# Performance work log

Hardware: AMD Instinct MI355X
Metric: run time of the kernel (lower is better)

The kernel has to match this reference:

```python
import jax, jax.numpy as jnp
import numpy as np

N_NODES = 100000
N_EDGES = 3200000
N_GRAPHS = 64
IN_DIM, OUT_DIM = 16, 3


def _gcn_layer(x, src, dst, ew, W, b, n):
    # PyG GCNConv with edge_weight: transform first, then normalized propagate
    # with added self-loops (weight 1.0). deg_i = sum_{e: dst=i} w_e + 1.
    xw = x @ W  # [N, out]
    deg = jax.ops.segment_sum(ew, dst, num_segments=n) + 1.0  # [N]
    dinv = jax.lax.rsqrt(deg)
    norm = dinv[src] * ew * dinv[dst]  # [E]
    agg = jax.ops.segment_sum(xw[src] * norm[:, None], dst, num_segments=n)
    # self-loop contribution: dinv_i * 1.0 * dinv_i = 1/deg_i
    return agg + xw * (1.0 / deg)[:, None] + b


def setup_inputs() -> dict:
    key = jax.random.key(0)
    ks = jax.random.split(key, 16)
    glorot = lambda k, fi, fo: jax.random.normal(k, (fi, fo), jnp.float32) * jnp.sqrt(2.0 / (fi + fo))
    return {
        "x": jax.random.normal(ks[0], (N_NODES, IN_DIM), jnp.float32),
        "edge_index": jax.random.randint(ks[1], (2, N_EDGES), 0, N_NODES, jnp.int32),
        "edge_attr": jax.random.uniform(ks[2], (N_EDGES,), jnp.float32),
        "batch": jnp.sort(jax.random.randint(ks[3], (N_NODES,), 0, N_GRAPHS, jnp.int32)),
        "W1": glorot(ks[4], IN_DIM, 16), "b1": jnp.zeros((16,), jnp.float32),
        "W2": glorot(ks[5], 16, 64),     "b2": jnp.zeros((64,), jnp.float32),
        "W3": glorot(ks[6], 64, 256),    "b3": jnp.zeros((256,), jnp.float32),
        "L1": glorot(ks[7], 256, 128),   "c1": jnp.zeros((128,), jnp.float32),
        "L2": glorot(ks[8], 128, 64),    "c2": jnp.zeros((64,), jnp.float32),
        "L3": glorot(ks[9], 64, OUT_DIM), "c3": jnp.zeros((OUT_DIM,), jnp.float32),
    }


def reference(x, edge_index, edge_attr, batch, W1, b1, W2, b2, W3, b3, L1, c1, L2, c2, L3, c3):
    src, dst = edge_index[0], edge_index[1]
    h = jax.nn.silu(_gcn_layer(x, src, dst, edge_attr, W1, b1, N_NODES))
    h = jax.nn.silu(_gcn_layer(h, src, dst, edge_attr, W2, b2, N_NODES))
    h = jax.nn.silu(_gcn_layer(h, src, dst, edge_attr, W3, b3, N_NODES))
    # global mean pool per graph
    sums = jax.ops.segment_sum(h, batch, num_segments=N_GRAPHS)  # [G, 256]
    cnt = jax.ops.segment_sum(jnp.ones((N_NODES,), h.dtype), batch, num_segments=N_GRAPHS)
    pooled = sums / jnp.maximum(cnt, 1.0)[:, None]
    z = jax.nn.silu(pooled @ L1 + c1)
    z = jax.nn.silu(z @ L2 + c2)
    z = z @ L3 + c3
    return jnp.squeeze(z)
```

## Files before the change

### kernel.cpp

```cpp
#include <hip/hip_runtime.h>
#include <math.h>


#define NBH 1024
#define POOL_C 8
#define CAP 10240

typedef _Float16 half8 __attribute__((ext_vector_type(8)));
typedef float f32x4 __attribute__((ext_vector_type(4)));

__device__ __forceinline__ float silu_f(float v) { return v / (1.0f + expf(-v)); }

__global__ void k_init(const int* __restrict__ batch, int* __restrict__ bounds,
                       int* __restrict__ btotal, int N, int G) {
    int t = threadIdx.x;
    btotal[t] = 0;
    if (t > G) return;
    if (t == G) { bounds[G] = N; return; }
    int lo = 0, hi = N;
    while (lo < hi) { int m = (lo + hi) >> 1; if (batch[m] < t) lo = m + 1; else hi = m; }
    bounds[t] = lo;
}

__global__ __launch_bounds__(256) void k_bscatter(const int* __restrict__ src,
                                                  const int* __restrict__ dst,
                                                  const float* __restrict__ ew,
                                                  int* __restrict__ btotal,
                                                  int2* __restrict__ ebuf,
                                                  int E, int B, int ept) {
    __shared__ int hist[512];
    __shared__ int cur[512];
    int blk = blockIdx.x, t = threadIdx.x;
    for (int i = t; i < B; i += 256) hist[i] = 0;
    __syncthreads();
    int start = blk * 256 * ept;
    for (int j = 0; j < ept; j++) {
        int e = start + j * 256 + t;
        if (e < E) atomicAdd(&hist[dst[e] >> 8], 1);
    }
    __syncthreads();
    for (int b = t; b < B; b += 256)
        cur[b] = b * CAP + atomicAdd(&btotal[b], hist[b]);
    __syncthreads();
    for (int j = 0; j < ept; j++) {
        int e = start + j * 256 + t;
        if (e < E) {
            int d = dst[e];
            int b = d >> 8;
            int pos = atomicAdd(&cur[b], 1);
            if (pos < (b + 1) * CAP)
                ebuf[pos] = make_int2(src[e] | ((d & 255) << 24), __float_as_int(ew[e]));
        }
    }
}

__global__ __launch_bounds__(256) void k_bucket_csr(const int2* __restrict__ ebuf,
                                                    const int* __restrict__ btotal,
                                                    int2* __restrict__ csr,
                                                    unsigned int* __restrict__ offs,
                                                    float* __restrict__ dinv,
                                                    const float* __restrict__ x,
                                                    _Float16* __restrict__ xp,
                                                    int N) {
    __shared__ int ncnt[256];
    __shared__ int excl[256];
    __shared__ float wsum[256];
    int b = blockIdx.x, t = threadIdx.x;
    int base = b * CAP;
    int end = base + min(btotal[b], CAP);
    ncnt[t] = 0;
    wsum[t] = 0.0f;
    __syncthreads();
    for (int i = base + t; i < end; i += 256)
        atomicAdd(&ncnt[(unsigned)ebuf[i].x >> 24], 1);
    __syncthreads();
    int v = ncnt[t];
    excl[t] = v;
    __syncthreads();
#pragma unroll
    for (int o = 1; o < 256; o <<= 1) {
        int x2 = (t >= o) ? excl[t - o] : 0;
        __syncthreads();
        excl[t] += x2;
        __syncthreads();
    }
    int ex = excl[t] - v;
    int n = (b << 8) + t;
    if (n < N) offs[n] = (unsigned)(base + ex) | ((unsigned)v << 24);
    __syncthreads();
    ncnt[t] = base + ex;
    __syncthreads();
    for (int i = base + t; i < end; i += 256) {
        int2 ent = ebuf[i];
        int node = (unsigned)ent.x >> 24;
        int pos = atomicAdd(&ncnt[node], 1);
        csr[pos] = make_int2(ent.x & 0x00FFFFFF, ent.y);
        atomicAdd(&wsum[node], __int_as_float(ent.y));
    }
    __syncthreads();
    if (n < N) {
        float dv = 1.0f / sqrtf(1.0f + wsum[t]);
        dinv[n] = dv;
        const float4* xr = (const float4*)(x + (long long)n * 16);
        half8* xw = (half8*)(xp + (long long)n * 16);
#pragma unroll
        for (int j = 0; j < 2; j++) {
            float4 a = xr[2 * j], c = xr[2 * j + 1];
            half8 hv;
            hv[0] = (_Float16)(a.x * dv); hv[1] = (_Float16)(a.y * dv);
            hv[2] = (_Float16)(a.z * dv); hv[3] = (_Float16)(a.w * dv);
            hv[4] = (_Float16)(c.x * dv); hv[5] = (_Float16)(c.y * dv);
            hv[6] = (_Float16)(c.z * dv); hv[7] = (_Float16)(c.w * dv);
            xw[j] = hv;
        }
    }
}

__global__ __launch_bounds__(256) void k_gx1(const _Float16* __restrict__ h,
                                             const int2* __restrict__ csr,
                                             const unsigned int* __restrict__ offs,
                                             const float* __restrict__ dinv,
                                             const float* __restrict__ W,
                                             const float* __restrict__ b,
                                             _Float16* __restrict__ out, int N) {
    __shared__ float Ws[16 * 16];
    __shared__ float bs[16];
    if (threadIdx.x < 256) Ws[threadIdx.x] = W[threadIdx.x];
    if (threadIdx.x < 16) bs[threadIdx.x] = b[threadIdx.x];
    __syncthreads();
    int n = blockIdx.x * 4 + (threadIdx.x >> 6);
    n = __builtin_amdgcn_readfirstlane(n);
    if (n >= N) return;
    int lane = threadIdx.x & 63;
    int d = lane & 15, eg = lane >> 4;
    unsigned op = offs[n];
    int p0 = op & 0x00FFFFFF;
    int len = op >> 24;
    int qs = p0 + ((len * eg) >> 2);
    int qe = p0 + ((len * (eg + 1)) >> 2);
    float acc = 0.0f;
    int p = qs;
    for (; p + 7 < qe; p += 8) {
        int2 e0 = csr[p], e1 = csr[p + 1], e2 = csr[p + 2], e3 = csr[p + 3];
        int2 e4 = csr[p + 4], e5 = csr[p + 5], e6 = csr[p + 6], e7 = csr[p + 7];
        float v0 = (float)h[e0.x * 16 + d], v1 = (float)h[e1.x * 16 + d];
        float v2 = (float)h[e2.x * 16 + d], v3 = (float)h[e3.x * 16 + d];
        float v4 = (float)h[e4.x * 16 + d], v5 = (float)h[e5.x * 16 + d];
        float v6 = (float)h[e6.x * 16 + d], v7 = (float)h[e7.x * 16 + d];
        acc += __int_as_float(e0.y) * v0; acc += __int_as_float(e1.y) * v1;
        acc += __int_as_float(e2.y) * v2; acc += __int_as_float(e3.y) * v3;
        acc += __int_as_float(e4.y) * v4; acc += __int_as_float(e5.y) * v5;
        acc += __int_as_float(e6.y) * v6; acc += __int_as_float(e7.y) * v7;
    }
    if (p + 3 < qe) {
        int2 e0 = csr[p], e1 = csr[p + 1], e2 = csr[p + 2], e3 = csr[p + 3];
        float v0 = (float)h[e0.x * 16 + d], v1 = (float)h[e1.x * 16 + d];
        float v2 = (float)h[e2.x * 16 + d], v3 = (float)h[e3.x * 16 + d];
        acc += __int_as_float(e0.y) * v0; acc += __int_as_float(e1.y) * v1;
        acc += __int_as_float(e2.y) * v2; acc += __int_as_float(e3.y) * v3;
        p += 4;
    }
    if (p + 1 < qe) {
        int2 e0 = csr[p], e1 = csr[p + 1];
        acc += __int_as_float(e0.y) * (float)h[e0.x * 16 + d];
        acc += __int_as_float(e1.y) * (float)h[e1.x * 16 + d];
        p += 2;
    }
    if (p < qe) {
        int2 e0 = csr[p];
        acc += __int_as_float(e0.y) * (float)h[e0.x * 16 + d];
    }
    acc += __shfl_down(acc, 32, 64);
    acc += __shfl_down(acc, 16, 64);
    float dv = dinv[n];
    float yv = (acc + ((lane < 16) ? (float)h[n * 16 + lane] : 0.0f)) * dv;
    float o = bs[d];
#pragma unroll
    for (int k = 0; k < 16; k++) o += __shfl(yv, k, 64) * Ws[k * 16 + d];
    if (lane < 16) out[n * 16 + lane] = (_Float16)(silu_f(o) * dv);
}

__global__ __launch_bounds__(256) void k_gx2(const _Float16* __restrict__ h,
                                             const int2* __restrict__ csr,
                                             const unsigned int* __restrict__ offs,
                                             const float* __restrict__ dinv,
                                             const float* __restrict__ W,
                                             const float* __restrict__ b,
                                             _Float16* __restrict__ out, int N) {
    __shared__ float Ws[16 * 64];
    __shared__ float bs[64];
    for (int i = threadIdx.x; i < 16 * 64; i += 256) Ws[i] = W[i];
    if (threadIdx.x < 64) bs[threadIdx.x] = b[threadIdx.x];
    __syncthreads();
    int n = blockIdx.x * 4 + (threadIdx.x >> 6);
    n = __builtin_amdgcn_readfirstlane(n);
    if (n >= N) return;
    int lane = threadIdx.x & 63;
    int d = lane & 15, eg = lane >> 4;
    unsigned op = offs[n];
    int p0 = op & 0x00FFFFFF;
    int len = op >> 24;
    int qs = p0 + ((len * eg) >> 2);
    int qe = p0 + ((len * (eg + 1)) >> 2);
    float acc = 0.0f;
    int p = qs;
    for (; p + 7 < qe; p += 8) {
        int2 e0 = csr[p], e1 = csr[p + 1], e2 = csr[p + 2], e3 = csr[p + 3];
        int2 e4 = csr[p + 4], e5 = csr[p + 5], e6 = csr[p + 6], e7 = csr[p + 7];
        float v0 = (float)h[e0.x * 16 + d], v1 = (float)h[e1.x * 16 + d];
        float v2 = (float)h[e2.x * 16 + d], v3 = (float)h[e3.x * 16 + d];
        float v4 = (float)h[e4.x * 16 + d], v5 = (float)h[e5.x * 16 + d];
        float v6 = (float)h[e6.x * 16 + d], v7 = (float)h[e7.x * 16 + d];
        acc += __int_as_float(e0.y) * v0; acc += __int_as_float(e1.y) * v1;
        acc += __int_as_float(e2.y) * v2; acc += __int_as_float(e3.y) * v3;
        acc += __int_as_float(e4.y) * v4; acc += __int_as_float(e5.y) * v5;
        acc += __int_as_float(e6.y) * v6; acc += __int_as_float(e7.y) * v7;
    }
    if (p + 3 < qe) {
        int2 e0 = csr[p], e1 = csr[p + 1], e2 = csr[p + 2], e3 = csr[p + 3];
        float v0 = (float)h[e0.x * 16 + d], v1 = (float)h[e1.x * 16 + d];
        float v2 = (float)h[e2.x * 16 + d], v3 = (float)h[e3.x * 16 + d];
        acc += __int_as_float(e0.y) * v0; acc += __int_as_float(e1.y) * v1;
        acc += __int_as_float(e2.y) * v2; acc += __int_as_float(e3.y) * v3;
        p += 4;
    }
    if (p + 1 < qe) {
        int2 e0 = csr[p], e1 = csr[p + 1];
        acc += __int_as_float(e0.y) * (float)h[e0.x * 16 + d];
        acc += __int_as_float(e1.y) * (float)h[e1.x * 16 + d];
        p += 2;
    }
    if (p < qe) {
        int2 e0 = csr[p];
        acc += __int_as_float(e0.y) * (float)h[e0.x * 16 + d];
    }
    acc += __shfl_down(acc, 32, 64);
    acc += __shfl_down(acc, 16, 64);
    float dv = dinv[n];
    float yv = (acc + ((lane < 16) ? (float)h[n * 16 + lane] : 0.0f)) * dv;
    float o = bs[lane];
#pragma unroll
    for (int k = 0; k < 16; k++) o += __shfl(yv, k, 64) * Ws[k * 64 + lane];
    out[(long long)n * 64 + lane] = (_Float16)(silu_f(o) * dv);
}

__global__ __launch_bounds__(256) void k_gather64(const _Float16* __restrict__ h,
                                                  const int2* __restrict__ csr,
                                                  const unsigned int* __restrict__ offs,
                                                  const float* __restrict__ dinv,
                                                  _Float16* __restrict__ y, int N) {
    int n = blockIdx.x * 4 + (threadIdx.x >> 6);
    n = __builtin_amdgcn_readfirstlane(n);
    if (n >= N) return;
    int lane = threadIdx.x & 63;
    unsigned op = offs[n];
    const int2* row = csr + (op & 0x00FFFFFF);
    int len = op >> 24;
    float acc = 0.0f;
    int j = 0;
    for (; j + 7 < len; j += 8) {
        int2 ee[8];
        float vv[8];
#pragma unroll
        for (int i = 0; i < 8; i++) ee[i] = row[j + i];
#pragma unroll
        for (int i = 0; i < 8; i++) vv[i] = (float)h[ee[i].x * 64 + lane];
#pragma unroll
        for (int i = 0; i < 8; i++) acc += __int_as_float(ee[i].y) * vv[i];
    }
    if (j + 3 < len) {
        int2 e0 = row[j], e1 = row[j + 1], e2 = row[j + 2], e3 = row[j + 3];
        float v0 = (float)h[e0.x * 64 + lane];
        float v1 = (float)h[e1.x * 64 + lane];
        float v2 = (float)h[e2.x * 64 + lane];
        float v3 = (float)h[e3.x * 64 + lane];
        acc += __int_as_float(e0.y) * v0;
        acc += __int_as_float(e1.y) * v1;
        acc += __int_as_float(e2.y) * v2;
        acc += __int_as_float(e3.y) * v3;
        j += 4;
    }
    for (; j < len; j++) {
        int2 e0 = row[j];
        acc += __int_as_float(e0.y) * (float)h[e0.x * 64 + lane];
    }
    y[n * 64 + lane] = (_Float16)((acc + (float)h[n * 64 + lane]) * dinv[n]);
}

__global__ __launch_bounds__(256) void k_xform3pool(const _Float16* __restrict__ y,
                                                    const float* __restrict__ W,
                                                    const float* __restrict__ b,
                                                    const int* __restrict__ bounds,
                                                    float* __restrict__ partial,
                                                    int N) {
    int lane = threadIdx.x & 63;
    int wave = threadIdx.x >> 6;
    int g = blockIdx.x / POOL_C;
    int c = blockIdx.x % POOL_C;
    int s = bounds[g], e = bounds[g + 1];
    int len = e - s;
    int cs = s + (int)((long long)len * c / POOL_C);
    int ce = s + (int)((long long)len * (c + 1) / POOL_C);
    int lg = lane >> 4;
    int lr = lane & 15;

    half8 bf[4][2];
#pragma unroll
    for (int t = 0; t < 4; t++) {
        int col = (wave * 4 + t) * 16 + lr;
#pragma unroll
        for (int s2 = 0; s2 < 2; s2++) {
            half8 v;
#pragma unroll
            for (int j = 0; j < 8; j++)
                v[j] = (_Float16)W[(s2 * 32 + lg * 8 + j) * 256 + col];
            bf[t][s2] = v;
        }
    }
    float bias[4];
#pragma unroll
    for (int t = 0; t < 4; t++) bias[t] = b[(wave * 4 + t) * 16 + lr];

    float pacc[4] = {0.f, 0.f, 0.f, 0.f};

    for (int base = cs; base < ce; base += 16) {
        int node = base + lr;
        int cn = node < N ? node : N - 1;
        const half8* arow = (const half8*)(y + (long long)cn * 64);
        half8 a0 = arow[lg];
        half8 a1 = arow[4 + lg];
#pragma unroll
        for (int t = 0; t < 4; t++) {
            f32x4 acc = {0.f, 0.f, 0.f, 0.f};
            acc = __builtin_amdgcn_mfma_f32_16x16x32_f16(a0, bf[t][0], acc, 0, 0, 0);
            acc = __builtin_amdgcn_mfma_f32_16x16x32_f16(a1, bf[t][1], acc, 0, 0, 0);
#pragma unroll
            for (int r = 0; r < 4; r++) {
                int nrow = base + lg * 4 + r;
                if (nrow < ce) pacc[t] += silu_f(acc[r] + bias[t]);
            }
        }
    }
#pragma unroll
    for (int t = 0; t < 4; t++) {
        pacc[t] += __shfl_xor(pacc[t], 16, 64);
        pacc[t] += __shfl_xor(pacc[t], 32, 64);
    }
    if (lane < 16) {
        float* pr = partial + (long long)blockIdx.x * 256 + wave * 64;
#pragma unroll
        for (int t = 0; t < 4; t++) pr[t * 16 + lane] = pacc[t];
    }
}

__global__ __launch_bounds__(256) void k_mlp(const float* __restrict__ partial,
                                             const int* __restrict__ bounds,
                                             const float* __restrict__ L1,
                                             const float* __restrict__ c1,
                                             const float* __restrict__ L2,
                                             const float* __restrict__ c2,
                                             const float* __restrict__ L3,
                                             const float* __restrict__ c3,
                                             float* __restrict__ out) {
    __shared__ float pooled[256];
    __shared__ float z1[128];
    __shared__ float z2[64];
    int g = blockIdx.x;
    int t = threadIdx.x;
    int cnt = bounds[g + 1] - bounds[g];
    float s = 0.0f;
    for (int c = 0; c < POOL_C; c++) s += partial[((long long)g * POOL_C + c) * 256 + t];
    pooled[t] = s / (float)(cnt > 0 ? cnt : 1);
    __syncthreads();
    if (t < 128) {
        float acc = c1[t];
        for (int k = 0; k < 256; k++) acc += pooled[k] * L1[k * 128 + t];
        z1[t] = silu_f(acc);
    }
    __syncthreads();
    if (t < 64) {
        float acc = c2[t];
        for (int k = 0; k < 128; k++) acc += z1[k] * L2[k * 64 + t];
        z2[t] = silu_f(acc);
    }
    __syncthreads();
    if (t < 3) {
        float acc = c3[t];
        for (int k = 0; k < 64; k++) acc += z2[k] * L3[k * 3 + t];
        out[g * 3 + t] = acc;
    }
}

extern "C" void kernel_launch(void* const* d_in, const int* in_sizes, int n_in,
                              void* d_out, int out_size, void* d_ws, size_t ws_size,
                              hipStream_t stream) {
    const float* x     = (const float*)d_in[0];
    const int*   ei    = (const int*)d_in[1];
    const float* ea    = (const float*)d_in[2];
    const int*   batch = (const int*)d_in[3];
    const float* W1 = (const float*)d_in[4];
    const float* b1 = (const float*)d_in[5];
    const float* W2 = (const float*)d_in[6];
    const float* b2 = (const float*)d_in[7];
    const float* W3 = (const float*)d_in[8];
    const float* b3 = (const float*)d_in[9];
    const float* L1 = (const float*)d_in[10];
    const float* c1 = (const float*)d_in[11];
    const float* L2 = (const float*)d_in[12];
    const float* c2 = (const float*)d_in[13];
    const float* L3 = (const float*)d_in[14];
    const float* c3 = (const float*)d_in[15];
    float* out = (float*)d_out;

    const int N = in_sizes[0] / 16;
    const int E = in_sizes[2];
    const int G = out_size / 3;
    const int* src = ei;
    const int* dst = ei + E;
    const int B = (N + 255) >> 8;
    const int ept = (E + NBH * 256 - 1) / (NBH * 256);

    char* ws = (char*)d_ws;
    size_t off = 0;
    auto alloc = [&](size_t bytes) -> void* {
        void* p = (void*)(ws + off);
        off += (bytes + 255) & ~(size_t)255;
        return p;
    };
    float*        dinv    = (float*)alloc((size_t)N * 4);
    unsigned int* offs    = (unsigned int*)alloc((size_t)N * 4);
    int*          btotal  = (int*)  alloc(512 * 4);
    int*          bounds  = (int*)  alloc((size_t)(G + 1) * 4);
    int2*         ebuf    = (int2*) alloc((size_t)B * CAP * 8);
    int2*         csr     = (int2*) alloc((size_t)B * CAP * 8);
    _Float16*     xp      = (_Float16*)alloc((size_t)N * 16 * 2);
    _Float16*     h1s     = (_Float16*)alloc((size_t)N * 16 * 2);
    _Float16*     h2s     = (_Float16*)alloc((size_t)N * 64 * 2);
    _Float16*     y64     = (_Float16*)alloc((size_t)N * 64 * 2);
    float*        partial = (float*)alloc((size_t)G * POOL_C * 256 * 4);
    (void)ws_size;

    k_init<<<1, 512, 0, stream>>>(batch, bounds, btotal, N, G);
    k_bscatter<<<NBH, 256, 0, stream>>>(src, dst, ea, btotal, ebuf, E, B, ept);
    k_bucket_csr<<<B, 256, 0, stream>>>(ebuf, btotal, csr, offs, dinv, x, xp, N);

    k_gx1<<<(N + 3) / 4, 256, 0, stream>>>(xp, csr, offs, dinv, W1, b1, h1s, N);

    k_gx2<<<(N + 3) / 4, 256, 0, stream>>>(h1s, csr, offs, dinv, W2, b2, h2s, N);

    k_gather64<<<(N + 3) / 4, 256, 0, stream>>>(h2s, csr, offs, dinv, y64, N);
    k_xform3pool<<<G * POOL_C, 256, 0, stream>>>(y64, W3, b3, bounds, partial, N);

    k_mlp<<<G, 256, 0, stream>>>(partial, bounds, L1, c1, L2, c2, L3, c3, out);
}
```

Measured before the change: 430.1 us.

## Replace bucketed two-pass CSR build with global-atomic count and scatter

The CSR build no longer sorts edges into 256-node buckets in an intermediate buffer and then sorts each bucket in shared memory. It now counts in-degree and weight sum per node with global atomics, computes offsets per 256-node block, then scatters each edge straight to its CSR slot using a global atomic cursor per node. This removes the intermediate ebuf array and its extra read/write passes. In exchange it adds several million global atomics, including float atomics, and fully random CSR writes. The per-bucket overflow guard is now a single global limit, so an overfull bucket would write into the next bucket's region instead of being clipped.

```diff
diff --git a/kernel.cpp b/kernel.cpp
--- a/kernel.cpp
+++ b/kernel.cpp
@@ -2,7 +2,7 @@
 #include <math.h>
 
 
-#define NBH 1024
+#define NSC 2048
 #define POOL_C 8
 #define CAP 10240
 
@@ -11,70 +11,49 @@
 
 __device__ __forceinline__ float silu_f(float v) { return v / (1.0f + expf(-v)); }
 
-__global__ void k_init(const int* __restrict__ batch, int* __restrict__ bounds,
-                       int* __restrict__ btotal, int N, int G) {
-    int t = threadIdx.x;
-    btotal[t] = 0;
-    if (t > G) return;
-    if (t == G) { bounds[G] = N; return; }
-    int lo = 0, hi = N;
-    while (lo < hi) { int m = (lo + hi) >> 1; if (batch[m] < t) lo = m + 1; else hi = m; }
-    bounds[t] = lo;
-}
-
-__global__ __launch_bounds__(256) void k_bscatter(const int* __restrict__ src,
-                                                  const int* __restrict__ dst,
-                                                  const float* __restrict__ ew,
-                                                  int* __restrict__ btotal,
-                                                  int2* __restrict__ ebuf,
-                                                  int E, int B, int ept) {
-    __shared__ int hist[512];
-    __shared__ int cur[512];
-    int blk = blockIdx.x, t = threadIdx.x;
-    for (int i = t; i < B; i += 256) hist[i] = 0;
-    __syncthreads();
-    int start = blk * 256 * ept;
-    for (int j = 0; j < ept; j++) {
-        int e = start + j * 256 + t;
-        if (e < E) atomicAdd(&hist[dst[e] >> 8], 1);
-    }
-    __syncthreads();
-    for (int b = t; b < B; b += 256)
-        cur[b] = b * CAP + atomicAdd(&btotal[b], hist[b]);
-    __syncthreads();
-    for (int j = 0; j < ept; j++) {
-        int e = start + j * 256 + t;
-        if (e < E) {
-            int d = dst[e];
-            int b = d >> 8;
-            int pos = atomicAdd(&cur[b], 1);
-            if (pos < (b + 1) * CAP)
-                ebuf[pos] = make_int2(src[e] | ((d & 255) << 24), __float_as_int(ew[e]));
-        }
-    }
-}
-
-__global__ __launch_bounds__(256) void k_bucket_csr(const int2* __restrict__ ebuf,
-                                                    const int* __restrict__ btotal,
-                                                    int2* __restrict__ csr,
-                                                    unsigned int* __restrict__ offs,
-                                                    float* __restrict__ dinv,
-                                                    const float* __restrict__ x,
-                                                    _Float16* __restrict__ xp,
-                                                    int N) {
-    __shared__ int ncnt[256];
+__global__ __launch_bounds__(256) void k_init(const int* __restrict__ batch,
+                                              int* __restrict__ bounds,
+                                              int* __restrict__ ncnt,
+                                              float* __restrict__ wsum,
+                                              int N, int G) {
+    int i = blockIdx.x * 256 + threadIdx.x;
+    int stride = gridDim.x * 256;
+    for (int k = i; k < N; k += stride) { ncnt[k] = 0; wsum[k] = 0.0f; }
+    if (blockIdx.x == 0) {
+        int t = threadIdx.x;
+        if (t > G) return;
+        if (t == G) { bounds[G] = N; return; }
+        int lo = 0, hi = N;
+        while (lo < hi) { int m = (lo + hi) >> 1; if (batch[m] < t) lo = m + 1; else hi = m; }
+        bounds[t] = lo;
+    }
+}
+
+__global__ __launch_bounds__(256) void k_count(const int* __restrict__ dst,
+                                               const float* __restrict__ ew,
+                                               int* __restrict__ ncnt,
+                                               float* __restrict__ wsum, int E) {
+    int e = blockIdx.x * 256 + threadIdx.x;
+    int stride = gridDim.x * 256;
+    for (; e < E; e += stride) {
+        int d = dst[e];
+        atomicAdd(&ncnt[d], 1);
+        atomicAdd(&wsum[d], ew[e]);
+    }
+}
+
+__global__ __launch_bounds__(256) void k_nodeprep(const int* __restrict__ ncnt,
+                                                  const float* __restrict__ wsum,
+                                                  unsigned int* __restrict__ offs,
+                                                  int* __restrict__ curs,
+                                                  float* __restrict__ dinv,
+                                                  const float* __restrict__ x,
+                                                  _Float16* __restrict__ xp,
+                                                  int N) {
     __shared__ int excl[256];
-    __shared__ float wsum[256];
     int b = blockIdx.x, t = threadIdx.x;
-    int base = b * CAP;
-    int end = base + min(btotal[b], CAP);
-    ncnt[t] = 0;
-    wsum[t] = 0.0f;
-    __syncthreads();
-    for (int i = base + t; i < end; i += 256)
-        atomicAdd(&ncnt[(unsigned)ebuf[i].x >> 24], 1);
-    __syncthreads();
-    int v = ncnt[t];
+    int n = (b << 8) + t;
+    int v = (n < N) ? ncnt[n] : 0;
     excl[t] = v;
     __syncthreads();
 #pragma unroll
@@ -85,21 +64,11 @@
         __syncthreads();
     }
     int ex = excl[t] - v;
-    int n = (b << 8) + t;
-    if (n < N) offs[n] = (unsigned)(base + ex) | ((unsigned)v << 24);
-    __syncthreads();
-    ncnt[t] = base + ex;
-    __syncthreads();
-    for (int i = base + t; i < end; i += 256) {
-        int2 ent = ebuf[i];
-        int node = (unsigned)ent.x >> 24;
-        int pos = atomicAdd(&ncnt[node], 1);
-        csr[pos] = make_int2(ent.x & 0x00FFFFFF, ent.y);
-        atomicAdd(&wsum[node], __int_as_float(ent.y));
-    }
-    __syncthreads();
+    int base = b * CAP;
     if (n < N) {
-        float dv = 1.0f / sqrtf(1.0f + wsum[t]);
+        offs[n] = (unsigned)(base + ex) | ((unsigned)v << 24);
+        curs[n] = base + ex;
+        float dv = 1.0f / sqrtf(1.0f + wsum[n]);
         dinv[n] = dv;
         const float4* xr = (const float4*)(x + (long long)n * 16);
         half8* xw = (half8*)(xp + (long long)n * 16);
@@ -113,6 +82,22 @@
             hv[6] = (_Float16)(c.z * dv); hv[7] = (_Float16)(c.w * dv);
             xw[j] = hv;
         }
+    }
+}
+
+__global__ __launch_bounds__(256) void k_escatter(const int* __restrict__ src,
+                                                  const int* __restrict__ dst,
+                                                  const float* __restrict__ ew,
+                                                  int* __restrict__ curs,
+                                                  int2* __restrict__ csr,
+                                                  int E, int limit) {
+    int e = blockIdx.x * 256 + threadIdx.x;
+    int stride = gridDim.x * 256;
+    for (; e < E; e += stride) {
+        int d = dst[e];
+        int pos = atomicAdd(&curs[d], 1);
+        if (pos < limit)
+            csr[pos] = make_int2(src[e], __float_as_int(ew[e]));
     }
 }
 
@@ -418,7 +403,6 @@
     const int* src = ei;
     const int* dst = ei + E;
     const int B = (N + 255) >> 8;
-    const int ept = (E + NBH * 256 - 1) / (NBH * 256);
 
     char* ws = (char*)d_ws;
     size_t off = 0;
@@ -429,9 +413,10 @@
     };
     float*        dinv    = (float*)alloc((size_t)N * 4);
     unsigned int* offs    = (unsigned int*)alloc((size_t)N * 4);
-    int*          btotal  = (int*)  alloc(512 * 4);
+    int*          ncnt    = (int*)  alloc((size_t)N * 4);
+    float*        wsum    = (float*)alloc((size_t)N * 4);
+    int*          curs    = (int*)  alloc((size_t)N * 4);
     int*          bounds  = (int*)  alloc((size_t)(G + 1) * 4);
-    int2*         ebuf    = (int2*) alloc((size_t)B * CAP * 8);
     int2*         csr     = (int2*) alloc((size_t)B * CAP * 8);
     _Float16*     xp      = (_Float16*)alloc((size_t)N * 16 * 2);
     _Float16*     h1s     = (_Float16*)alloc((size_t)N * 16 * 2);
@@ -440,9 +425,10 @@
     float*        partial = (float*)alloc((size_t)G * POOL_C * 256 * 4);
     (void)ws_size;
 
-    k_init<<<1, 512, 0, stream>>>(batch, bounds, btotal, N, G);
-    k_bscatter<<<NBH, 256, 0, stream>>>(src, dst, ea, btotal, ebuf, E, B, ept);
-    k_bucket_csr<<<B, 256, 0, stream>>>(ebuf, btotal, csr, offs, dinv, x, xp, N);
+    k_init<<<256, 256, 0, stream>>>(batch, bounds, ncnt, wsum, N, G);
+    k_count<<<NSC, 256, 0, stream>>>(dst, ea, ncnt, wsum, E);
+    k_nodeprep<<<B, 256, 0, stream>>>(ncnt, wsum, offs, curs, dinv, x, xp, N);
+    k_escatter<<<NSC, 256, 0, stream>>>(src, dst, ea, curs, csr, E, B * CAP);
 
     k_gx1<<<(N + 3) / 4, 256, 0, stream>>>(xp, csr, offs, dinv, W1, b1, h1s, N);
 
```

New measurement: 866.6 us. +101.5%, slower.

## Pack CSR entries into 32 bits with 17-bit source and fp15 weight

Applied to the files above, without the earlier changes.

Each CSR entry shrinks from an int2 (src, fp32 weight) to a single 32-bit word. The source index goes in the upper 17 bits and the weight in the lower 15 bits as fp16 with the sign bit dropped, which assumes nonnegative weights. This halves the CSR bytes streamed by all three gather kernels and by the CSR build. It costs weight precision, drops the sign, and limits node ids to 131072, which covers the 100000 nodes here.

```diff
diff --git a/kernel.cpp b/kernel.cpp
--- a/kernel.cpp
+++ b/kernel.cpp
@@ -10,6 +10,20 @@
 typedef float f32x4 __attribute__((ext_vector_type(4)));
 
 __device__ __forceinline__ float silu_f(float v) { return v / (1.0f + expf(-v)); }
+
+__device__ __forceinline__ int psrc(unsigned u) { return (int)(u >> 15); }
+__device__ __forceinline__ float pew(unsigned u) {
+    unsigned short hs = (unsigned short)(u & 0x7FFFu);
+    _Float16 hv;
+    __builtin_memcpy(&hv, &hs, 2);
+    return (float)hv;
+}
+__device__ __forceinline__ unsigned packent(int src, float w) {
+    _Float16 hw = (_Float16)w;
+    unsigned short hb;
+    __builtin_memcpy(&hb, &hw, 2);
+    return ((unsigned)src << 15) | (unsigned)(hb & 0x7FFFu);
+}
 
 __global__ void k_init(const int* __restrict__ batch, int* __restrict__ bounds,
                        int* __restrict__ btotal, int N, int G) {
@@ -56,7 +70,7 @@
 
 __global__ __launch_bounds__(256) void k_bucket_csr(const int2* __restrict__ ebuf,
                                                     const int* __restrict__ btotal,
-                                                    int2* __restrict__ csr,
+                                                    unsigned int* __restrict__ csr,
                                                     unsigned int* __restrict__ offs,
                                                     float* __restrict__ dinv,
                                                     const float* __restrict__ x,
@@ -93,9 +107,10 @@
     for (int i = base + t; i < end; i += 256) {
         int2 ent = ebuf[i];
         int node = (unsigned)ent.x >> 24;
+        float w = __int_as_float(ent.y);
         int pos = atomicAdd(&ncnt[node], 1);
-        csr[pos] = make_int2(ent.x & 0x00FFFFFF, ent.y);
-        atomicAdd(&wsum[node], __int_as_float(ent.y));
+        csr[pos] = packent(ent.x & 0x00FFFFFF, w);
+        atomicAdd(&wsum[node], w);
     }
     __syncthreads();
     if (n < N) {
@@ -117,7 +132,7 @@
 }
 
 __global__ __launch_bounds__(256) void k_gx1(const _Float16* __restrict__ h,
-                                             const int2* __restrict__ csr,
+                                             const unsigned int* __restrict__ csr,
                                              const unsigned int* __restrict__ offs,
                                              const float* __restrict__ dinv,
                                              const float* __restrict__ W,
@@ -141,34 +156,32 @@
     float acc = 0.0f;
     int p = qs;
     for (; p + 7 < qe; p += 8) {
-        int2 e0 = csr[p], e1 = csr[p + 1], e2 = csr[p + 2], e3 = csr[p + 3];
-        int2 e4 = csr[p + 4], e5 = csr[p + 5], e6 = csr[p + 6], e7 = csr[p + 7];
-        float v0 = (float)h[e0.x * 16 + d], v1 = (float)h[e1.x * 16 + d];
-        float v2 = (float)h[e2.x * 16 + d], v3 = (float)h[e3.x * 16 + d];
-        float v4 = (float)h[e4.x * 16 + d], v5 = (float)h[e5.x * 16 + d];
-        float v6 = (float)h[e6.x * 16 + d], v7 = (float)h[e7.x * 16 + d];
-        acc += __int_as_float(e0.y) * v0; acc += __int_as_float(e1.y) * v1;
-        acc += __int_as_float(e2.y) * v2; acc += __int_as_float(e3.y) * v3;
-        acc += __int_as_float(e4.y) * v4; acc += __int_as_float(e5.y) * v5;
-        acc += __int_as_float(e6.y) * v6; acc += __int_as_float(e7.y) * v7;
+        unsigned ee[8];
+#pragma unroll
+        for (int i = 0; i < 8; i++) ee[i] = csr[p + i];
+        float vv[8];
+#pragma unroll
+        for (int i = 0; i < 8; i++) vv[i] = (float)h[psrc(ee[i]) * 16 + d];
+#pragma unroll
+        for (int i = 0; i < 8; i++) acc += pew(ee[i]) * vv[i];
     }
     if (p + 3 < qe) {
-        int2 e0 = csr[p], e1 = csr[p + 1], e2 = csr[p + 2], e3 = csr[p + 3];
-        float v0 = (float)h[e0.x * 16 + d], v1 = (float)h[e1.x * 16 + d];
-        float v2 = (float)h[e2.x * 16 + d], v3 = (float)h[e3.x * 16 + d];
-        acc += __int_as_float(e0.y) * v0; acc += __int_as_float(e1.y) * v1;
-        acc += __int_as_float(e2.y) * v2; acc += __int_as_float(e3.y) * v3;
+        unsigned e0 = csr[p], e1 = csr[p + 1], e2 = csr[p + 2], e3 = csr[p + 3];
+        float v0 = (float)h[psrc(e0) * 16 + d], v1 = (float)h[psrc(e1) * 16 + d];
+        float v2 = (float)h[psrc(e2) * 16 + d], v3 = (float)h[psrc(e3) * 16 + d];
+        acc += pew(e0) * v0; acc += pew(e1) * v1;
+        acc += pew(e2) * v2; acc += pew(e3) * v3;
         p += 4;
     }
     if (p + 1 < qe) {
-        int2 e0 = csr[p], e1 = csr[p + 1];
-        acc += __int_as_float(e0.y) * (float)h[e0.x * 16 + d];
-        acc += __int_as_float(e1.y) * (float)h[e1.x * 16 + d];
+        unsigned e0 = csr[p], e1 = csr[p + 1];
+        acc += pew(e0) * (float)h[psrc(e0) * 16 + d];
+        acc += pew(e1) * (float)h[psrc(e1) * 16 + d];
         p += 2;
     }
     if (p < qe) {
-        int2 e0 = csr[p];
-        acc += __int_as_float(e0.y) * (float)h[e0.x * 16 + d];
+        unsigned e0 = csr[p];
+        acc += pew(e0) * (float)h[psrc(e0) * 16 + d];
     }
     acc += __shfl_down(acc, 32, 64);
     acc += __shfl_down(acc, 16, 64);
@@ -181,7 +194,7 @@
 }
 
 __global__ __launch_bounds__(256) void k_gx2(const _Float16* __restrict__ h,
-                                             const int2* __restrict__ csr,
+                                             const unsigned int* __restrict__ csr,
                                              const unsigned int* __restrict__ offs,
                                              const float* __restrict__ dinv,
                                              const float* __restrict__ W,
@@ -205,34 +218,32 @@
     float acc = 0.0f;
     int p = qs;
     for (; p + 7 < qe; p += 8) {
-        int2 e0 = csr[p], e1 = csr[p + 1], e2 = csr[p + 2], e3 = csr[p + 3];
-        int2 e4 = csr[p + 4], e5 = csr[p + 5], e6 = csr[p + 6], e7 = csr[p + 7];
-        float v0 = (float)h[e0.x * 16 + d], v1 = (float)h[e1.x * 16 + d];
-        float v2 = (float)h[e2.x * 16 + d], v3 = (float)h[e3.x * 16 + d];
-        float v4 = (float)h[e4.x * 16 + d], v5 = (float)h[e5.x * 16 + d];
-        float v6 = (float)h[e6.x * 16 + d], v7 = (float)h[e7.x * 16 + d];
-        acc += __int_as_float(e0.y) * v0; acc += __int_as_float(e1.y) * v1;
-        acc += __int_as_float(e2.y) * v2; acc += __int_as_float(e3.y) * v3;
-        acc += __int_as_float(e4.y) * v4; acc += __int_as_float(e5.y) * v5;
-        acc += __int_as_float(e6.y) * v6; acc += __int_as_float(e7.y) * v7;
+        unsigned ee[8];
+#pragma unroll
+        for (int i = 0; i < 8; i++) ee[i] = csr[p + i];
+        float vv[8];
+#pragma unroll
+        for (int i = 0; i < 8; i++) vv[i] = (float)h[psrc(ee[i]) * 16 + d];
+#pragma unroll
+        for (int i = 0; i < 8; i++) acc += pew(ee[i]) * vv[i];
     }
     if (p + 3 < qe) {
-        int2 e0 = csr[p], e1 = csr[p + 1], e2 = csr[p + 2], e3 = csr[p + 3];
-        float v0 = (float)h[e0.x * 16 + d], v1 = (float)h[e1.x * 16 + d];
-        float v2 = (float)h[e2.x * 16 + d], v3 = (float)h[e3.x * 16 + d];
-        acc += __int_as_float(e0.y) * v0; acc += __int_as_float(e1.y) * v1;
-        acc += __int_as_float(e2.y) * v2; acc += __int_as_float(e3.y) * v3;
+        unsigned e0 = csr[p], e1 = csr[p + 1], e2 = csr[p + 2], e3 = csr[p + 3];
+        float v0 = (float)h[psrc(e0) * 16 + d], v1 = (float)h[psrc(e1) * 16 + d];
+        float v2 = (float)h[psrc(e2) * 16 + d], v3 = (float)h[psrc(e3) * 16 + d];
+        acc += pew(e0) * v0; acc += pew(e1) * v1;
+        acc += pew(e2) * v2; acc += pew(e3) * v3;
         p += 4;
     }
     if (p + 1 < qe) {
-        int2 e0 = csr[p], e1 = csr[p + 1];
-        acc += __int_as_float(e0.y) * (float)h[e0.x * 16 + d];
-        acc += __int_as_float(e1.y) * (float)h[e1.x * 16 + d];
+        unsigned e0 = csr[p], e1 = csr[p + 1];
+        acc += pew(e0) * (float)h[psrc(e0) * 16 + d];
+        acc += pew(e1) * (float)h[psrc(e1) * 16 + d];
         p += 2;
     }
     if (p < qe) {
-        int2 e0 = csr[p];
-        acc += __int_as_float(e0.y) * (float)h[e0.x * 16 + d];
+        unsigned e0 = csr[p];
+        acc += pew(e0) * (float)h[psrc(e0) * 16 + d];
     }
     acc += __shfl_down(acc, 32, 64);
     acc += __shfl_down(acc, 16, 64);
@@ -245,7 +256,7 @@
 }
 
 __global__ __launch_bounds__(256) void k_gather64(const _Float16* __restrict__ h,
-                                                  const int2* __restrict__ csr,
+                                                  const unsigned int* __restrict__ csr,
                                                   const unsigned int* __restrict__ offs,
                                                   const float* __restrict__ dinv,
                                                   _Float16* __restrict__ y, int N) {
@@ -254,35 +265,35 @@
     if (n >= N) return;
     int lane = threadIdx.x & 63;
     unsigned op = offs[n];
-    const int2* row = csr + (op & 0x00FFFFFF);
+    const unsigned* row = csr + (op & 0x00FFFFFF);
     int len = op >> 24;
     float acc = 0.0f;
     int j = 0;
     for (; j + 7 < len; j += 8) {
-        int2 ee[8];
+        unsigned ee[8];
         float vv[8];
 #pragma unroll
         for (int i = 0; i < 8; i++) ee[i] = row[j + i];
 #pragma unroll
-        for (int i = 0; i < 8; i++) vv[i] = (float)h[ee[i].x * 64 + lane];
-#pragma unroll
-        for (int i = 0; i < 8; i++) acc += __int_as_float(ee[i].y) * vv[i];
+        for (int i = 0; i < 8; i++) vv[i] = (float)h[psrc(ee[i]) * 64 + lane];
+#pragma unroll
+        for (int i = 0; i < 8; i++) acc += pew(ee[i]) * vv[i];
     }
     if (j + 3 < len) {
-        int2 e0 = row[j], e1 = row[j + 1], e2 = row[j + 2], e3 = row[j + 3];
-        float v0 = (float)h[e0.x * 64 + lane];
-        float v1 = (float)h[e1.x * 64 + lane];
-        float v2 = (float)h[e2.x * 64 + lane];
-        float v3 = (float)h[e3.x * 64 + lane];
-        acc += __int_as_float(e0.y) * v0;
-        acc += __int_as_float(e1.y) * v1;
-        acc += __int_as_float(e2.y) * v2;
-        acc += __int_as_float(e3.y) * v3;
+        unsigned e0 = row[j], e1 = row[j + 1], e2 = row[j + 2], e3 = row[j + 3];
+        float v0 = (float)h[psrc(e0) * 64 + lane];
+        float v1 = (float)h[psrc(e1) * 64 + lane];
+        float v2 = (float)h[psrc(e2) * 64 + lane];
+        float v3 = (float)h[psrc(e3) * 64 + lane];
+        acc += pew(e0) * v0;
+        acc += pew(e1) * v1;
+        acc += pew(e2) * v2;
+        acc += pew(e3) * v3;
         j += 4;
     }
     for (; j < len; j++) {
-        int2 e0 = row[j];
-        acc += __int_as_float(e0.y) * (float)h[e0.x * 64 + lane];
+        unsigned e0 = row[j];
+        acc += pew(e0) * (float)h[psrc(e0) * 64 + lane];
     }
     y[n * 64 + lane] = (_Float16)((acc + (float)h[n * 64 + lane]) * dinv[n]);
 }
@@ -432,7 +443,7 @@
     int*          btotal  = (int*)  alloc(512 * 4);
     int*          bounds  = (int*)  alloc((size_t)(G + 1) * 4);
     int2*         ebuf    = (int2*) alloc((size_t)B * CAP * 8);
-    int2*         csr     = (int2*) alloc((size_t)B * CAP * 8);
+    unsigned int* csr     = (unsigned int*)alloc((size_t)B * CAP * 4);
     _Float16*     xp      = (_Float16*)alloc((size_t)N * 16 * 2);
     _Float16*     h1s     = (_Float16*)alloc((size_t)N * 16 * 2);
     _Float16*     h2s     = (_Float16*)alloc((size_t)N * 64 * 2);
```

Result: no change. 426.9 us (-0.7%).
